# Kernel tuning notes

Hardware: AMD Instinct MI355X
Metric: run time of the kernel (lower is better)

## Reference

```python
import jax, jax.numpy as jnp
import numpy as np

C = 512
K = 3
DIL = 1
EPS = 1e-6


def weight_quant(w):
    # BitNet b1.58 ternary quantization with straight-through estimator:
    # scale = mean(|w|); w_q = clamp(round(w/scale), -1, 1) * scale
    s = jnp.maximum(jnp.mean(jnp.abs(w)), 1e-5)
    q = jnp.clip(jnp.round(w / s), -1.0, 1.0) * s
    return w + jax.lax.stop_gradient(q - w)


def conv1d(x, w, b, padding, dilation):
    # x: [B, C, L], w: [O, I, K]
    y = jax.lax.conv_general_dilated(
        x, w, window_strides=(1,), padding=[(padding, padding)],
        rhs_dilation=(dilation,), dimension_numbers=("NCH", "OIH", "NCH"))
    return y + b[None, :, None]


def setup_inputs() -> dict:
    key = jax.random.key(0)
    k0, k1, k2, k3, k4 = jax.random.split(key, 5)
    fan_in = C * K
    lim = 1.0 / np.sqrt(fan_in)
    x = jax.random.normal(k0, (16, C, 4096), dtype=jnp.float32)
    w1 = jax.random.uniform(k1, (C, C, K), jnp.float32, -lim, lim)
    b1 = jax.random.uniform(k2, (C,), jnp.float32, -lim, lim)
    w2 = jax.random.uniform(k3, (C, C, K), jnp.float32, -lim, lim)
    b2 = jax.random.uniform(k4, (C,), jnp.float32, -lim, lim)
    g = jnp.ones((C,), dtype=jnp.float32)  # RMSNorm gain
    return {"x": x, "w1": w1, "b1": b1, "w2": w2, "b2": b2, "g": g}


def reference(x, w1, b1, w2, b2, g):
    residual = x
    # RMSNorm over channel axis (original transposes to [B,L,C], norms last dim)
    ms = jnp.mean(jnp.square(x), axis=1, keepdims=True)
    h = x * jax.lax.rsqrt(ms + EPS) * g[None, :, None]
    h = jax.nn.silu(h)
    p1 = (K * DIL - DIL) // 2
    h = conv1d(h, weight_quant(w1), b1, p1, DIL)
    h = jax.nn.silu(h)
    h = conv1d(h, weight_quant(w2), b2, K // 2, 1)
    return h + residual
```

## Files before the change

kernel.cpp:

```cpp
#include <hip/hip_runtime.h>

#define BATCH 16
#define CCH 512
#define LEN 4096
#define LPAD 4098

typedef unsigned short u16;
typedef __bf16 bf16x8 __attribute__((ext_vector_type(8)));
typedef float f32x4 __attribute__((ext_vector_type(4)));
typedef u16 u16x8 __attribute__((ext_vector_type(8)));
typedef u16 u16x4 __attribute__((ext_vector_type(4)));

__device__ __forceinline__ u16 f2bf(float f) {
    unsigned u = __float_as_uint(f);
    u = (u + 0x7fffu + ((u >> 16) & 1u)) >> 16;
    return (u16)u;
}
__device__ __forceinline__ float bf2f(u16 v) {
    return __uint_as_float(((unsigned)v) << 16);
}
__device__ __forceinline__ float silu_f(float v) {
    return v / (1.f + __expf(-v));
}
__device__ __forceinline__ void async16(const u16* g, u16* l) {
    __builtin_amdgcn_global_load_lds(
        (const __attribute__((address_space(1))) unsigned int*)g,
        (__attribute__((address_space(3))) unsigned int*)l, 16, 0, 0);
}

#define SBAR() __builtin_amdgcn_sched_barrier(0)
#define HWBAR() { SBAR(); __builtin_amdgcn_s_barrier(); SBAR(); }
#define WAIT_LGKM0() { asm volatile("s_waitcnt lgkmcnt(0)" ::: "memory"); SBAR(); }
#define WAIT_VM(n) { asm volatile("s_waitcnt vmcnt(" #n ")" ::: "memory"); SBAR(); }

__global__ __launch_bounds__(256)
void absmean_partial(const float* __restrict__ w1, const float* __restrict__ w2,
                     float* __restrict__ part) {
    const int tid = threadIdx.x;
    const int base = blockIdx.x * 3072;
    float s1 = 0.f, s2 = 0.f;
    for (int i = tid; i < 3072; i += 256) {
        s1 += fabsf(w1[base + i]);
        s2 += fabsf(w2[base + i]);
    }
    __shared__ float r1[256], r2[256];
    r1[tid] = s1; r2[tid] = s2;
    __syncthreads();
    for (int off = 128; off > 0; off >>= 1) {
        if (tid < off) { r1[tid] += r1[tid + off]; r2[tid] += r2[tid + off]; }
        __syncthreads();
    }
    if (tid == 0) { part[blockIdx.x] = r1[0]; part[256 + blockIdx.x] = r2[0]; }
}

__global__ __launch_bounds__(256)
void finalize_scale(const float* __restrict__ part, float* __restrict__ sv) {
    const int tid = threadIdx.x;
    __shared__ float r1[256], r2[256];
    r1[tid] = part[tid]; r2[tid] = part[256 + tid];
    __syncthreads();
    for (int off = 128; off > 0; off >>= 1) {
        if (tid < off) { r1[tid] += r1[tid + off]; r2[tid] += r2[tid + off]; }
        __syncthreads();
    }
    if (tid == 0) {
        sv[0] = fmaxf(r1[0] * (1.f / 786432.f), 1e-5f);
        sv[1] = fmaxf(r2[0] * (1.f / 786432.f), 1e-5f);
    }
}

__global__ __launch_bounds__(256)
void quantize_w(const float* __restrict__ w, const float* __restrict__ sv,
                int sidx, u16* __restrict__ wqt) {
    const int idx = blockIdx.x * 256 + threadIdx.x;
    const float s = sv[sidx];
    float q = rintf(w[idx] / s);
    q = fmaxf(-1.f, fminf(1.f, q));
    const int o   = idx / 1536;
    const int rem = idx - o * 1536;
    const int i   = rem / 3;
    const int k   = rem - i * 3;
    wqt[k * (CCH * CCH) + o * CCH + i] = f2bf(q);
}

__global__ __launch_bounds__(256)
void zero_pads(u16* __restrict__ h, u16* __restrict__ h1) {
    const int idx = blockIdx.x * 256 + threadIdx.x;
    const int b = idx >> 10;
    const int r = (idx >> 9) & 1;
    const int i = idx & 511;
    const size_t off = ((size_t)b * LPAD + (r ? (LPAD - 1) : 0)) * CCH + i;
    h[off] = 0;
    h1[off] = 0;
}

__global__ __launch_bounds__(256)
void rms_silu_transpose(const float* __restrict__ x, const float* __restrict__ g,
                        u16* __restrict__ h_t) {
    __shared__ u16   xt[CCH][33];
    __shared__ float red[8][32];
    __shared__ float rinv[32];
    const int tid = threadIdx.x;
    const int bb  = blockIdx.x >> 7;
    const int l0  = (blockIdx.x & 127) << 5;

    const size_t xbase = (size_t)bb * CCH * LEN + l0;
    {
        const int i_hi = tid >> 3;
        const int l4   = (tid & 7) << 2;
        #pragma unroll
        for (int it = 0; it < 16; ++it) {
            const int i = it * 32 + i_hi;
            const float4 v = *(const float4*)&x[xbase + (size_t)i * LEN + l4];
            xt[i][l4 + 0] = f2bf(v.x);
            xt[i][l4 + 1] = f2bf(v.y);
            xt[i][l4 + 2] = f2bf(v.z);
            xt[i][l4 + 3] = f2bf(v.w);
        }
    }
    __syncthreads();
    {
        const int l = tid & 31, seg = tid >> 5;
        const int ibeg = seg * 64;
        float ss = 0.f;
        #pragma unroll 8
        for (int i = ibeg; i < ibeg + 64; ++i) {
            const float v = bf2f(xt[i][l]);
            ss += v * v;
        }
        red[seg][l] = ss;
    }
    __syncthreads();
    if (tid < 32) {
        float tot = 0.f;
        #pragma unroll
        for (int k2 = 0; k2 < 8; ++k2) tot += red[k2][tid];
        rinv[tid] = rsqrtf(tot * (1.f / 512.f) + 1e-6f);
    }
    __syncthreads();
    {
        const int l  = tid >> 3;
        const int i0 = (tid & 7) << 6;
        const float ri = rinv[l];
        const size_t ob = ((size_t)bb * LPAD + l0 + l + 1) * CCH + i0;
        for (int ii = 0; ii < 64; ii += 8) {
            u16x8 ov;
            #pragma unroll
            for (int jj = 0; jj < 8; ++jj) {
                const int i = i0 + ii + jj;
                float v = bf2f(xt[i][l]) * ri * g[i];
                ov[jj] = f2bf(silu_f(v));
            }
            *(u16x8*)&h_t[ob + ii] = ov;
        }
    }
}

template<int EPI>
__global__ __launch_bounds__(1024)
void conv_gemm8(const u16* __restrict__ Bsrc, const u16* __restrict__ Wq,
                const float* __restrict__ sptr, const float* __restrict__ bias,
                const float* __restrict__ resid, u16* __restrict__ outb,
                float* __restrict__ outf) {
    extern __shared__ u16 lds[];
    const int tid  = threadIdx.x;
    const int lane = tid & 63;
    const int wave = tid >> 6;
    const int wm = wave >> 2;
    const int wn = wave & 3;

    const int wgid = (blockIdx.x & 7) * 64 + (blockIdx.x >> 3);
    const int mt = wgid & 1;
    const int nt = wgid >> 1;
    const int o0 = mt << 8;
    const int bb = nt >> 4;
    const int l0 = (nt & 15) << 8;

    const int sr  = tid >> 3;
    const int scu = ((tid & 7) << 3) ^ ((sr & 7) << 3);
    const int sdst = tid << 3;

    const u16* aSrcBase = Wq + (size_t)o0 * CCH + scu;
    const u16* bSrcBase = Bsrc + ((size_t)bb * LPAD + l0) * CCH + scu;

    auto stage_full = [&](int pb, int ks2, int i02) {
        #pragma unroll
        for (int j = 0; j < 2; ++j) {
            const int r = j * 128 + sr;
            async16(aSrcBase + ks2 * (CCH * CCH) + r * CCH + i02,
                    &lds[pb * 32768 + j * 8192 + sdst]);
            async16(bSrcBase + (size_t)(r + ks2) * CCH + i02,
                    &lds[pb * 32768 + 16384 + j * 8192 + sdst]);
        }
    };

    const int swz = (lane & 7) << 3;
    const int c0 = ((lane >> 4) << 3) ^ swz;
    const int c1 = (((lane >> 4) << 3) + 32) ^ swz;
    const int aB = wm * 4096 + (lane & 15) * 64;
    const int bB = 16384 + wn * 4096 + (lane & 15) * 64;

    f32x4 acc[4][4];
    #pragma unroll
    for (int m = 0; m < 4; ++m)
        #pragma unroll
        for (int n = 0; n < 4; ++n)
            acc[m][n] = (f32x4){0.f, 0.f, 0.f, 0.f};

    stage_full(0, 0, 0);
    WAIT_VM(0);
    HWBAR();

    for (int t = 0; t < 24; ++t) {
        const int cur = t & 1;
        const int cbase = cur * 32768;
        if (t + 1 < 24) {
            const int tn = t + 1;
            stage_full(cur ^ 1, tn % 3, (tn / 3) << 6);
        }
        #pragma unroll
        for (int kk = 0; kk < 2; ++kk) {
            const int ck = kk ? c1 : c0;
            bf16x8 ar[4], br[4];
            #pragma unroll
            for (int m = 0; m < 4; ++m)
                ar[m] = *(const bf16x8*)&lds[cbase + aB + m * 1024 + ck];
            #pragma unroll
            for (int n = 0; n < 4; ++n)
                br[n] = *(const bf16x8*)&lds[cbase + bB + n * 1024 + ck];
            __builtin_amdgcn_s_setprio(1);
            #pragma unroll
            for (int m = 0; m < 4; ++m)
                #pragma unroll
                for (int n = 0; n < 4; ++n)
                    acc[m][n] = __builtin_amdgcn_mfma_f32_16x16x32_bf16(
                        ar[m], br[n], acc[m][n], 0, 0, 0);
            __builtin_amdgcn_s_setprio(0);
        }
        WAIT_LGKM0();
        WAIT_VM(0);
        HWBAR();
    }

    const float sc = sptr[0];

    if (EPI == 1) {
        #pragma unroll
        for (int m = 0; m < 4; ++m) {
            const int o_loc = wm * 64 + m * 16 + ((lane >> 4) << 2);
            const int ob = o0 + o_loc;
            const float b0 = bias[ob + 0], b1 = bias[ob + 1];
            const float b2 = bias[ob + 2], b3 = bias[ob + 3];
            #pragma unroll
            for (int n = 0; n < 4; ++n) {
                const int l_loc = wn * 64 + n * 16 + (lane & 15);
                const f32x4 a = acc[m][n];
                u16x4 ov;
                ov[0] = f2bf(silu_f(sc * a[0] + b0));
                ov[1] = f2bf(silu_f(sc * a[1] + b1));
                ov[2] = f2bf(silu_f(sc * a[2] + b2));
                ov[3] = f2bf(silu_f(sc * a[3] + b3));
                char* p = (char*)lds + l_loc * 512 +
                          (((unsigned)(o_loc << 1)) ^ ((l_loc & 7) << 4));
                *(u16x4*)p = ov;
            }
        }
        __syncthreads();
        const int l_r = tid >> 2;
        const int oq  = (tid & 3) << 3;
        u16* gdst = outb + ((size_t)bb * LPAD + l0 + l_r + 1) * CCH + o0 + oq;
        char* srp = (char*)lds + l_r * 512;
        const int swz2 = (l_r & 7) << 4;
        #pragma unroll
        for (int c = 0; c < 8; ++c) {
            const uint4 v = *(const uint4*)(srp + (((oq << 1) + c * 64) ^ swz2));
            *(uint4*)(gdst + c * 32) = v;
        }
    } else {
        const int lbase = l0 + wn * 64 + (lane & 15);
        const int obase = o0 + wm * 64 + ((lane >> 4) << 2);
        #pragma unroll
        for (int m = 0; m < 4; ++m) {
            const int ob = obase + m * 16;
            #pragma unroll
            for (int n = 0; n < 4; ++n) {
                const int l = lbase + n * 16;
                const f32x4 a = acc[m][n];
                #pragma unroll
                for (int jj = 0; jj < 4; ++jj) {
                    const size_t idx = ((size_t)bb * CCH + (ob + jj)) * LEN + l;
                    outf[idx] = sc * a[jj] + bias[ob + jj] + resid[idx];
                }
            }
        }
    }
}

extern "C" void kernel_launch(void* const* d_in, const int* in_sizes, int n_in,
                              void* d_out, int out_size, void* d_ws, size_t ws_size,
                              hipStream_t stream) {
    const float* x  = (const float*)d_in[0];
    const float* w1 = (const float*)d_in[1];
    const float* b1 = (const float*)d_in[2];
    const float* w2 = (const float*)d_in[3];
    const float* b2 = (const float*)d_in[4];
    const float* g  = (const float*)d_in[5];
    float* out = (float*)d_out;

    char* ws = (char*)d_ws;
    float* sv   = (float*)ws;
    float* part = (float*)(ws + 256);
    u16* wq1   = (u16*)(ws + 4096);
    u16* wq2   = (u16*)(ws + 4096 + 1572864);
    u16* h_t   = (u16*)(ws + 4096 + 2 * 1572864);
    u16* h1_t  = (u16*)(ws + 4096 + 2 * 1572864 + 67141632);

    hipFuncSetAttribute((const void*)conv_gemm8<1>,
                        hipFuncAttributeMaxDynamicSharedMemorySize, 131072);
    hipFuncSetAttribute((const void*)conv_gemm8<2>,
                        hipFuncAttributeMaxDynamicSharedMemorySize, 131072);

    absmean_partial<<<dim3(256), dim3(256), 0, stream>>>(w1, w2, part);
    finalize_scale<<<dim3(1), dim3(256), 0, stream>>>(part, sv);
    quantize_w<<<dim3(3072), dim3(256), 0, stream>>>(w1, sv, 0, wq1);
    quantize_w<<<dim3(3072), dim3(256), 0, stream>>>(w2, sv, 1, wq2);
    zero_pads<<<dim3(64), dim3(256), 0, stream>>>(h_t, h1_t);
    rms_silu_transpose<<<dim3(2048), dim3(256), 0, stream>>>(x, g, h_t);
    conv_gemm8<1><<<dim3(512), dim3(1024), 131072, stream>>>(h_t, wq1, sv, b1,
                                                             nullptr, h1_t, nullptr);
    conv_gemm8<2><<<dim3(512), dim3(1024), 131072, stream>>>(h1_t, wq2, sv + 1, b2,
                                                             x, nullptr, out);
}
```

Measured before the change: 306.9 us.

## Shrink conv GEMM tile to 256x128 with 3-stage async LDS pipeline

Both conv GEMM launches move from 1024-thread blocks computing 256x256 output tiles with double-buffered 64-wide K slices to 512-thread blocks computing 256x128 tiles. These now use 32-wide K slices in a triple-buffered ring, with loads issued two steps ahead. The LDS swizzle and staging pattern are rewritten to match. Dynamic LDS drops so more blocks can be resident per CU and load latency is better hidden. In exchange there are twice as many barriers per block and less operand reuse per tile.

```diff
diff --git a/kernel.cpp b/kernel.cpp
--- a/kernel.cpp
+++ b/kernel.cpp
@@ -157,7 +157,7 @@
 }
 
 template<int EPI>
-__global__ __launch_bounds__(1024)
+__global__ __launch_bounds__(512)
 void conv_gemm8(const u16* __restrict__ Bsrc, const u16* __restrict__ Wq,
                 const float* __restrict__ sptr, const float* __restrict__ bias,
                 const float* __restrict__ resid, u16* __restrict__ outb,
@@ -166,39 +166,35 @@
     const int tid  = threadIdx.x;
     const int lane = tid & 63;
     const int wave = tid >> 6;
-    const int wm = wave >> 2;
-    const int wn = wave & 3;
-
-    const int wgid = (blockIdx.x & 7) * 64 + (blockIdx.x >> 3);
+    const int wm = wave >> 1;
+    const int wn = wave & 1;
+
+    const int wgid = (blockIdx.x & 7) * 128 + (blockIdx.x >> 3);
     const int mt = wgid & 1;
     const int nt = wgid >> 1;
     const int o0 = mt << 8;
-    const int bb = nt >> 4;
-    const int l0 = (nt & 15) << 8;
-
-    const int sr  = tid >> 3;
-    const int scu = ((tid & 7) << 3) ^ ((sr & 7) << 3);
+    const int bb = nt >> 5;
+    const int l0 = (nt & 31) << 7;
+
+    const int sr   = tid >> 2;
+    const int scol = ((tid & 3) << 3) ^ ((sr & 3) << 3);
     const int sdst = tid << 3;
 
-    const u16* aSrcBase = Wq + (size_t)o0 * CCH + scu;
-    const u16* bSrcBase = Bsrc + ((size_t)bb * LPAD + l0) * CCH + scu;
-
-    auto stage_full = [&](int pb, int ks2, int i02) {
-        #pragma unroll
-        for (int j = 0; j < 2; ++j) {
-            const int r = j * 128 + sr;
-            async16(aSrcBase + ks2 * (CCH * CCH) + r * CCH + i02,
-                    &lds[pb * 32768 + j * 8192 + sdst]);
-            async16(bSrcBase + (size_t)(r + ks2) * CCH + i02,
-                    &lds[pb * 32768 + 16384 + j * 8192 + sdst]);
-        }
+    const u16* aSrcBase = Wq + (size_t)(o0 + sr) * CCH + scol;
+    const u16* bSrcBase = Bsrc + ((size_t)bb * LPAD + l0 + sr) * CCH + scol;
+
+    auto stage_full = [&](int pb, int t) {
+        const int ks = t % 3;
+        const int i0 = (t / 3) << 5;
+        const u16* wsrc = aSrcBase + ks * (CCH * CCH) + i0;
+        async16(wsrc, &lds[pb * 12288 + sdst]);
+        async16(wsrc + 128 * CCH, &lds[pb * 12288 + 4096 + sdst]);
+        async16(bSrcBase + (size_t)ks * CCH + i0, &lds[pb * 12288 + 8192 + sdst]);
     };
 
-    const int swz = (lane & 7) << 3;
-    const int c0 = ((lane >> 4) << 3) ^ swz;
-    const int c1 = (((lane >> 4) << 3) + 32) ^ swz;
-    const int aB = wm * 4096 + (lane & 15) * 64;
-    const int bB = 16384 + wn * 4096 + (lane & 15) * 64;
+    const int cc = (((lane >> 4) ^ (lane & 3)) << 3);
+    const int aOff = (wm * 64 + (lane & 15)) * 32 + cc;
+    const int bOff = 8192 + (wn * 64 + (lane & 15)) * 32 + cc;
 
     f32x4 acc[4][4];
     #pragma unroll
@@ -207,39 +203,35 @@
         for (int n = 0; n < 4; ++n)
             acc[m][n] = (f32x4){0.f, 0.f, 0.f, 0.f};
 
-    stage_full(0, 0, 0);
-    WAIT_VM(0);
+    stage_full(0, 0);
+    stage_full(1, 1);
+    WAIT_VM(3);
     HWBAR();
 
-    for (int t = 0; t < 24; ++t) {
-        const int cur = t & 1;
-        const int cbase = cur * 32768;
-        if (t + 1 < 24) {
-            const int tn = t + 1;
-            stage_full(cur ^ 1, tn % 3, (tn / 3) << 6);
-        }
-        #pragma unroll
-        for (int kk = 0; kk < 2; ++kk) {
-            const int ck = kk ? c1 : c0;
-            bf16x8 ar[4], br[4];
-            #pragma unroll
-            for (int m = 0; m < 4; ++m)
-                ar[m] = *(const bf16x8*)&lds[cbase + aB + m * 1024 + ck];
+    int pb = 0;
+    for (int t = 0; t < 48; ++t) {
+        const int cb = pb * 12288;
+        const bool full = (t < 46);
+        if (full) stage_full((pb + 2) % 3, t + 2);
+        bf16x8 ar[4], br[4];
+        #pragma unroll
+        for (int m = 0; m < 4; ++m)
+            ar[m] = *(const bf16x8*)&lds[cb + aOff + m * 512];
+        #pragma unroll
+        for (int n = 0; n < 4; ++n)
+            br[n] = *(const bf16x8*)&lds[cb + bOff + n * 512];
+        __builtin_amdgcn_s_setprio(1);
+        #pragma unroll
+        for (int m = 0; m < 4; ++m)
             #pragma unroll
             for (int n = 0; n < 4; ++n)
-                br[n] = *(const bf16x8*)&lds[cbase + bB + n * 1024 + ck];
-            __builtin_amdgcn_s_setprio(1);
-            #pragma unroll
-            for (int m = 0; m < 4; ++m)
-                #pragma unroll
-                for (int n = 0; n < 4; ++n)
-                    acc[m][n] = __builtin_amdgcn_mfma_f32_16x16x32_bf16(
-                        ar[m], br[n], acc[m][n], 0, 0, 0);
-            __builtin_amdgcn_s_setprio(0);
-        }
+                acc[m][n] = __builtin_amdgcn_mfma_f32_16x16x32_bf16(
+                    ar[m], br[n], acc[m][n], 0, 0, 0);
+        __builtin_amdgcn_s_setprio(0);
         WAIT_LGKM0();
-        WAIT_VM(0);
+        if (full) { WAIT_VM(3); } else { WAIT_VM(0); }
         HWBAR();
+        pb = (pb + 1) % 3;
     }
 
     const float sc = sptr[0];
@@ -316,9 +308,9 @@
     u16* h1_t  = (u16*)(ws + 4096 + 2 * 1572864 + 67141632);
 
     hipFuncSetAttribute((const void*)conv_gemm8<1>,
-                        hipFuncAttributeMaxDynamicSharedMemorySize, 131072);
+                        hipFuncAttributeMaxDynamicSharedMemorySize, 73728);
     hipFuncSetAttribute((const void*)conv_gemm8<2>,
-                        hipFuncAttributeMaxDynamicSharedMemorySize, 131072);
+                        hipFuncAttributeMaxDynamicSharedMemorySize, 73728);
 
     absmean_partial<<<dim3(256), dim3(256), 0, stream>>>(w1, w2, part);
     finalize_scale<<<dim3(1), dim3(256), 0, stream>>>(part, sv);
@@ -326,8 +318,8 @@
     quantize_w<<<dim3(3072), dim3(256), 0, stream>>>(w2, sv, 1, wq2);
     zero_pads<<<dim3(64), dim3(256), 0, stream>>>(h_t, h1_t);
     rms_silu_transpose<<<dim3(2048), dim3(256), 0, stream>>>(x, g, h_t);
-    conv_gemm8<1><<<dim3(512), dim3(1024), 131072, stream>>>(h_t, wq1, sv, b1,
-                                                             nullptr, h1_t, nullptr);
-    conv_gemm8<2><<<dim3(512), dim3(1024), 131072, stream>>>(h1_t, wq2, sv + 1, b2,
-                                                             x, nullptr, out);
-}
+    conv_gemm8<1><<<dim3(1024), dim3(512), 73728, stream>>>(h_t, wq1, sv, b1,
+                                                            nullptr, h1_t, nullptr);
+    conv_gemm8<2><<<dim3(1024), dim3(512), 73728, stream>>>(h1_t, wq2, sv + 1, b2,
+                                                            x, nullptr, out);
+}
```

After: 328.8 us. +7.1%, slower.

## Load weight fragments directly from global and enlarge per-wave output tile

Applied to the files above, without the earlier changes.

The conv GEMM now runs 512-thread blocks (8 waves in a 4x2 grid), and each wave computes a 64x128 tile with 32 accumulators instead of 16. The weight (A) operand is no longer staged through LDS. Each lane reads its bf16 fragments straight from global or L2 every step, and only the activation (B) tile is double-buffered in LDS. The goal is to cut LDS traffic and A-staging work and raise MFMA density per wave. The cost is higher register pressure (128 accumulator floats plus 8 B fragments) and exposed global-load latency on the A path, while the dynamic LDS request stays at 128KB.

```diff
diff --git a/kernel.cpp b/kernel.cpp
--- a/kernel.cpp
+++ b/kernel.cpp
@@ -157,8 +157,8 @@
 }
 
 template<int EPI>
-__global__ __launch_bounds__(1024)
-void conv_gemm8(const u16* __restrict__ Bsrc, const u16* __restrict__ Wq,
+__global__ __launch_bounds__(512, 2)
+void conv_gemm9(const u16* __restrict__ Bsrc, const u16* __restrict__ Wq,
                 const float* __restrict__ sptr, const float* __restrict__ bias,
                 const float* __restrict__ resid, u16* __restrict__ outb,
                 float* __restrict__ outf) {
@@ -166,8 +166,8 @@
     const int tid  = threadIdx.x;
     const int lane = tid & 63;
     const int wave = tid >> 6;
-    const int wm = wave >> 2;
-    const int wn = wave & 3;
+    const int wm = wave >> 1;
+    const int wn = wave & 1;
 
     const int wgid = (blockIdx.x & 7) * 64 + (blockIdx.x >> 3);
     const int mt = wgid & 1;
@@ -179,67 +179,68 @@
     const int sr  = tid >> 3;
     const int scu = ((tid & 7) << 3) ^ ((sr & 7) << 3);
     const int sdst = tid << 3;
-
-    const u16* aSrcBase = Wq + (size_t)o0 * CCH + scu;
-    const u16* bSrcBase = Bsrc + ((size_t)bb * LPAD + l0) * CCH + scu;
-
-    auto stage_full = [&](int pb, int ks2, int i02) {
-        #pragma unroll
-        for (int j = 0; j < 2; ++j) {
-            const int r = j * 128 + sr;
-            async16(aSrcBase + ks2 * (CCH * CCH) + r * CCH + i02,
-                    &lds[pb * 32768 + j * 8192 + sdst]);
-            async16(bSrcBase + (size_t)(r + ks2) * CCH + i02,
-                    &lds[pb * 32768 + 16384 + j * 8192 + sdst]);
-        }
+    const u16* bSrcBase = Bsrc + ((size_t)bb * LPAD + l0 + sr) * CCH + scu;
+
+    auto stageB = [&](int pb, int ks2, int i02) {
+        #pragma unroll
+        for (int j = 0; j < 4; ++j)
+            async16(bSrcBase + (size_t)(j * 64 + ks2) * CCH + i02,
+                    &lds[pb * 16384 + j * 4096 + sdst]);
     };
+
+    const u16* aLane = Wq + ((size_t)(o0 + wm * 64 + (lane & 15)) << 9) +
+                       ((lane >> 4) << 3);
 
     const int swz = (lane & 7) << 3;
     const int c0 = ((lane >> 4) << 3) ^ swz;
     const int c1 = (((lane >> 4) << 3) + 32) ^ swz;
-    const int aB = wm * 4096 + (lane & 15) * 64;
-    const int bB = 16384 + wn * 4096 + (lane & 15) * 64;
-
-    f32x4 acc[4][4];
+    const int bOffBase = (wn * 128 + (lane & 15)) * 64;
+
+    f32x4 acc[4][8];
     #pragma unroll
     for (int m = 0; m < 4; ++m)
         #pragma unroll
-        for (int n = 0; n < 4; ++n)
+        for (int n = 0; n < 8; ++n)
             acc[m][n] = (f32x4){0.f, 0.f, 0.f, 0.f};
 
-    stage_full(0, 0, 0);
+    stageB(0, 0, 0);
     WAIT_VM(0);
     HWBAR();
 
+    int ks = 0, i0 = 0;
     for (int t = 0; t < 24; ++t) {
-        const int cur = t & 1;
-        const int cbase = cur * 32768;
-        if (t + 1 < 24) {
-            const int tn = t + 1;
-            stage_full(cur ^ 1, tn % 3, (tn / 3) << 6);
-        }
+        const int pb = t & 1;
+        const u16* aT = aLane + ks * (CCH * CCH) + i0;
+        bf16x8 aA[4][2];
+        #pragma unroll
+        for (int m = 0; m < 4; ++m) {
+            aA[m][0] = *(const bf16x8*)(aT + m * 8192);
+            aA[m][1] = *(const bf16x8*)(aT + m * 8192 + 32);
+        }
+        int ksn = ks + 1, i0n = i0;
+        if (ksn == 3) { ksn = 0; i0n += 64; }
+        if (t < 23) stageB(pb ^ 1, ksn, i0n);
+        const int cb = pb * 16384;
         #pragma unroll
         for (int kk = 0; kk < 2; ++kk) {
             const int ck = kk ? c1 : c0;
-            bf16x8 ar[4], br[4];
-            #pragma unroll
-            for (int m = 0; m < 4; ++m)
-                ar[m] = *(const bf16x8*)&lds[cbase + aB + m * 1024 + ck];
-            #pragma unroll
-            for (int n = 0; n < 4; ++n)
-                br[n] = *(const bf16x8*)&lds[cbase + bB + n * 1024 + ck];
+            bf16x8 br[8];
+            #pragma unroll
+            for (int n = 0; n < 8; ++n)
+                br[n] = *(const bf16x8*)&lds[cb + bOffBase + n * 1024 + ck];
             __builtin_amdgcn_s_setprio(1);
             #pragma unroll
             for (int m = 0; m < 4; ++m)
                 #pragma unroll
-                for (int n = 0; n < 4; ++n)
+                for (int n = 0; n < 8; ++n)
                     acc[m][n] = __builtin_amdgcn_mfma_f32_16x16x32_bf16(
-                        ar[m], br[n], acc[m][n], 0, 0, 0);
+                        aA[m][kk], br[n], acc[m][n], 0, 0, 0);
             __builtin_amdgcn_s_setprio(0);
         }
         WAIT_LGKM0();
         WAIT_VM(0);
         HWBAR();
+        ks = ksn; i0 = i0n;
     }
 
     const float sc = sptr[0];
@@ -252,8 +253,8 @@
             const float b0 = bias[ob + 0], b1 = bias[ob + 1];
             const float b2 = bias[ob + 2], b3 = bias[ob + 3];
             #pragma unroll
-            for (int n = 0; n < 4; ++n) {
-                const int l_loc = wn * 64 + n * 16 + (lane & 15);
+            for (int n = 0; n < 8; ++n) {
+                const int l_loc = wn * 128 + n * 16 + (lane & 15);
                 const f32x4 a = acc[m][n];
                 u16x4 ov;
                 ov[0] = f2bf(silu_f(sc * a[0] + b0));
@@ -268,22 +269,26 @@
         __syncthreads();
         const int l_r = tid >> 2;
         const int oq  = (tid & 3) << 3;
-        u16* gdst = outb + ((size_t)bb * LPAD + l0 + l_r + 1) * CCH + o0 + oq;
-        char* srp = (char*)lds + l_r * 512;
-        const int swz2 = (l_r & 7) << 4;
-        #pragma unroll
-        for (int c = 0; c < 8; ++c) {
-            const uint4 v = *(const uint4*)(srp + (((oq << 1) + c * 64) ^ swz2));
-            *(uint4*)(gdst + c * 32) = v;
+        #pragma unroll
+        for (int pass = 0; pass < 2; ++pass) {
+            const int lr = l_r + pass * 128;
+            u16* gdst = outb + ((size_t)bb * LPAD + l0 + lr + 1) * CCH + o0 + oq;
+            char* srp = (char*)lds + lr * 512;
+            const int swz2 = (lr & 7) << 4;
+            #pragma unroll
+            for (int c = 0; c < 8; ++c) {
+                const uint4 v = *(const uint4*)(srp + (((oq << 1) + c * 64) ^ swz2));
+                *(uint4*)(gdst + c * 32) = v;
+            }
         }
     } else {
-        const int lbase = l0 + wn * 64 + (lane & 15);
+        const int lbase = l0 + wn * 128 + (lane & 15);
         const int obase = o0 + wm * 64 + ((lane >> 4) << 2);
         #pragma unroll
         for (int m = 0; m < 4; ++m) {
             const int ob = obase + m * 16;
             #pragma unroll
-            for (int n = 0; n < 4; ++n) {
+            for (int n = 0; n < 8; ++n) {
                 const int l = lbase + n * 16;
                 const f32x4 a = acc[m][n];
                 #pragma unroll
@@ -315,9 +320,9 @@
     u16* h_t   = (u16*)(ws + 4096 + 2 * 1572864);
     u16* h1_t  = (u16*)(ws + 4096 + 2 * 1572864 + 67141632);
 
-    hipFuncSetAttribute((const void*)conv_gemm8<1>,
+    hipFuncSetAttribute((const void*)conv_gemm9<1>,
                         hipFuncAttributeMaxDynamicSharedMemorySize, 131072);
-    hipFuncSetAttribute((const void*)conv_gemm8<2>,
+    hipFuncSetAttribute((const void*)conv_gemm9<2>,
                         hipFuncAttributeMaxDynamicSharedMemorySize, 131072);
 
     absmean_partial<<<dim3(256), dim3(256), 0, stream>>>(w1, w2, part);
@@ -326,8 +331,8 @@
     quantize_w<<<dim3(3072), dim3(256), 0, stream>>>(w2, sv, 1, wq2);
     zero_pads<<<dim3(64), dim3(256), 0, stream>>>(h_t, h1_t);
     rms_silu_transpose<<<dim3(2048), dim3(256), 0, stream>>>(x, g, h_t);
-    conv_gemm8<1><<<dim3(512), dim3(1024), 131072, stream>>>(h_t, wq1, sv, b1,
-                                                             nullptr, h1_t, nullptr);
-    conv_gemm8<2><<<dim3(512), dim3(1024), 131072, stream>>>(h1_t, wq2, sv + 1, b2,
-                                                             x, nullptr, out);
-}
+    conv_gemm9<1><<<dim3(512), dim3(512), 131072, stream>>>(h_t, wq1, sv, b1,
+                                                            nullptr, h1_t, nullptr);
+    conv_gemm9<2><<<dim3(512), dim3(512), 131072, stream>>>(h1_t, wq2, sv + 1, b2,
+                                                            x, nullptr, out);
+}
```

New measurement: 442.2 us. 1.44x slower.

## Switch conv GEMM to 32x32x16 MFMA tiles and fuse weight quantization launches

Applied to the files above, without the earlier changes.

The conv GEMM inner loop now uses 32x32x16 bf16 MFMA with a 2x2 f32x16 accumulator per wave instead of a 4x4 grid of 16x16x32 MFMAs. This changes the LDS fragment load pattern and both epilogue index mappings. The larger instruction is meant to cut LDS reads per FLOP and the MFMA issue count. The two weight-quantization kernels are also merged into one launch. The risks are different LDS bank-conflict behaviour under the existing swizzle and a less coalesced fp32 output store in the second epilogue.

```diff
diff --git a/kernel.cpp b/kernel.cpp
--- a/kernel.cpp
+++ b/kernel.cpp
@@ -8,6 +8,7 @@
 typedef unsigned short u16;
 typedef __bf16 bf16x8 __attribute__((ext_vector_type(8)));
 typedef float f32x4 __attribute__((ext_vector_type(4)));
+typedef float f32x16 __attribute__((ext_vector_type(16)));
 typedef u16 u16x8 __attribute__((ext_vector_type(8)));
 typedef u16 u16x4 __attribute__((ext_vector_type(4)));
 
@@ -70,17 +71,20 @@
 }
 
 __global__ __launch_bounds__(256)
-void quantize_w(const float* __restrict__ w, const float* __restrict__ sv,
-                int sidx, u16* __restrict__ wqt) {
+void quantize_both(const float* __restrict__ w1, const float* __restrict__ w2,
+                   const float* __restrict__ sv,
+                   u16* __restrict__ wq1, u16* __restrict__ wq2) {
     const int idx = blockIdx.x * 256 + threadIdx.x;
-    const float s = sv[sidx];
-    float q = rintf(w[idx] / s);
-    q = fmaxf(-1.f, fminf(1.f, q));
+    const float s1 = sv[0], s2 = sv[1];
     const int o   = idx / 1536;
     const int rem = idx - o * 1536;
     const int i   = rem / 3;
     const int k   = rem - i * 3;
-    wqt[k * (CCH * CCH) + o * CCH + i] = f2bf(q);
+    const int dst = k * (CCH * CCH) + o * CCH + i;
+    float q1 = fmaxf(-1.f, fminf(1.f, rintf(w1[idx] / s1)));
+    float q2 = fmaxf(-1.f, fminf(1.f, rintf(w2[idx] / s2)));
+    wq1[dst] = f2bf(q1);
+    wq2[dst] = f2bf(q2);
 }
 
 __global__ __launch_bounds__(256)
@@ -158,10 +162,10 @@
 
 template<int EPI>
 __global__ __launch_bounds__(1024)
-void conv_gemm8(const u16* __restrict__ Bsrc, const u16* __restrict__ Wq,
-                const float* __restrict__ sptr, const float* __restrict__ bias,
-                const float* __restrict__ resid, u16* __restrict__ outb,
-                float* __restrict__ outf) {
+void conv_gemm10(const u16* __restrict__ Bsrc, const u16* __restrict__ Wq,
+                 const float* __restrict__ sptr, const float* __restrict__ bias,
+                 const float* __restrict__ resid, u16* __restrict__ outb,
+                 float* __restrict__ outf) {
     extern __shared__ u16 lds[];
     const int tid  = threadIdx.x;
     const int lane = tid & 63;
@@ -195,74 +199,76 @@
     };
 
     const int swz = (lane & 7) << 3;
-    const int c0 = ((lane >> 4) << 3) ^ swz;
-    const int c1 = (((lane >> 4) << 3) + 32) ^ swz;
-    const int aB = wm * 4096 + (lane & 15) * 64;
-    const int bB = 16384 + wn * 4096 + (lane & 15) * 64;
-
-    f32x4 acc[4][4];
+    const int kb  = (lane >> 5) << 3;
+    const int aRowB = (wm * 64 + (lane & 31)) * 64;
+    const int bRowB = 16384 + (wn * 64 + (lane & 31)) * 64;
+
+    f32x16 acc[2][2];
     #pragma unroll
-    for (int m = 0; m < 4; ++m)
-        #pragma unroll
-        for (int n = 0; n < 4; ++n)
-            acc[m][n] = (f32x4){0.f, 0.f, 0.f, 0.f};
+    for (int m = 0; m < 2; ++m)
+        #pragma unroll
+        for (int n = 0; n < 2; ++n)
+            acc[m][n] = (f32x16){0.f,0.f,0.f,0.f,0.f,0.f,0.f,0.f,
+                                 0.f,0.f,0.f,0.f,0.f,0.f,0.f,0.f};
 
     stage_full(0, 0, 0);
     WAIT_VM(0);
     HWBAR();
 
+    int ks = 0, i0 = 0;
     for (int t = 0; t < 24; ++t) {
         const int cur = t & 1;
         const int cbase = cur * 32768;
-        if (t + 1 < 24) {
-            const int tn = t + 1;
-            stage_full(cur ^ 1, tn % 3, (tn / 3) << 6);
-        }
-        #pragma unroll
-        for (int kk = 0; kk < 2; ++kk) {
-            const int ck = kk ? c1 : c0;
-            bf16x8 ar[4], br[4];
-            #pragma unroll
-            for (int m = 0; m < 4; ++m)
-                ar[m] = *(const bf16x8*)&lds[cbase + aB + m * 1024 + ck];
-            #pragma unroll
-            for (int n = 0; n < 4; ++n)
-                br[n] = *(const bf16x8*)&lds[cbase + bB + n * 1024 + ck];
+        int ksn = ks + 1, i0n = i0;
+        if (ksn == 3) { ksn = 0; i0n += 64; }
+        if (t < 23) stage_full(cur ^ 1, ksn, i0n);
+        #pragma unroll
+        for (int s = 0; s < 4; ++s) {
+            const int ck = (s * 16 + kb) ^ swz;
+            bf16x8 av[2], bv[2];
+            #pragma unroll
+            for (int m = 0; m < 2; ++m)
+                av[m] = *(const bf16x8*)&lds[cbase + aRowB + m * 2048 + ck];
+            #pragma unroll
+            for (int n = 0; n < 2; ++n)
+                bv[n] = *(const bf16x8*)&lds[cbase + bRowB + n * 2048 + ck];
             __builtin_amdgcn_s_setprio(1);
             #pragma unroll
-            for (int m = 0; m < 4; ++m)
+            for (int m = 0; m < 2; ++m)
                 #pragma unroll
-                for (int n = 0; n < 4; ++n)
-                    acc[m][n] = __builtin_amdgcn_mfma_f32_16x16x32_bf16(
-                        ar[m], br[n], acc[m][n], 0, 0, 0);
+                for (int n = 0; n < 2; ++n)
+                    acc[m][n] = __builtin_amdgcn_mfma_f32_32x32x16_bf16(
+                        av[m], bv[n], acc[m][n], 0, 0, 0);
             __builtin_amdgcn_s_setprio(0);
         }
         WAIT_LGKM0();
         WAIT_VM(0);
         HWBAR();
+        ks = ksn; i0 = i0n;
     }
 
     const float sc = sptr[0];
+    const int hi = lane >> 5;
 
     if (EPI == 1) {
         #pragma unroll
-        for (int m = 0; m < 4; ++m) {
-            const int o_loc = wm * 64 + m * 16 + ((lane >> 4) << 2);
-            const int ob = o0 + o_loc;
-            const float b0 = bias[ob + 0], b1 = bias[ob + 1];
-            const float b2 = bias[ob + 2], b3 = bias[ob + 3];
-            #pragma unroll
-            for (int n = 0; n < 4; ++n) {
-                const int l_loc = wn * 64 + n * 16 + (lane & 15);
-                const f32x4 a = acc[m][n];
-                u16x4 ov;
-                ov[0] = f2bf(silu_f(sc * a[0] + b0));
-                ov[1] = f2bf(silu_f(sc * a[1] + b1));
-                ov[2] = f2bf(silu_f(sc * a[2] + b2));
-                ov[3] = f2bf(silu_f(sc * a[3] + b3));
-                char* p = (char*)lds + l_loc * 512 +
-                          (((unsigned)(o_loc << 1)) ^ ((l_loc & 7) << 4));
-                *(u16x4*)p = ov;
+        for (int m = 0; m < 2; ++m) {
+            #pragma unroll
+            for (int n = 0; n < 2; ++n) {
+                const int l_loc = wn * 64 + n * 32 + (lane & 31);
+                const f32x16 a = acc[m][n];
+                #pragma unroll
+                for (int q = 0; q < 4; ++q) {
+                    const int o_loc = wm * 64 + m * 32 + q * 8 + hi * 4;
+                    const int ob = o0 + o_loc;
+                    u16x4 ov;
+                    #pragma unroll
+                    for (int j = 0; j < 4; ++j)
+                        ov[j] = f2bf(silu_f(sc * a[q * 4 + j] + bias[ob + j]));
+                    char* p = (char*)lds + l_loc * 512 +
+                              (((unsigned)(o_loc << 1)) ^ ((l_loc & 7) << 4));
+                    *(u16x4*)p = ov;
+                }
             }
         }
         __syncthreads();
@@ -277,19 +283,20 @@
             *(uint4*)(gdst + c * 32) = v;
         }
     } else {
-        const int lbase = l0 + wn * 64 + (lane & 15);
-        const int obase = o0 + wm * 64 + ((lane >> 4) << 2);
-        #pragma unroll
-        for (int m = 0; m < 4; ++m) {
-            const int ob = obase + m * 16;
-            #pragma unroll
-            for (int n = 0; n < 4; ++n) {
-                const int l = lbase + n * 16;
-                const f32x4 a = acc[m][n];
+        #pragma unroll
+        for (int m = 0; m < 2; ++m) {
+            #pragma unroll
+            for (int n = 0; n < 2; ++n) {
+                const int l = l0 + wn * 64 + n * 32 + (lane & 31);
+                const f32x16 a = acc[m][n];
                 #pragma unroll
-                for (int jj = 0; jj < 4; ++jj) {
-                    const size_t idx = ((size_t)bb * CCH + (ob + jj)) * LEN + l;
-                    outf[idx] = sc * a[jj] + bias[ob + jj] + resid[idx];
+                for (int q = 0; q < 4; ++q) {
+                    const int ob = o0 + wm * 64 + m * 32 + q * 8 + hi * 4;
+                    #pragma unroll
+                    for (int j = 0; j < 4; ++j) {
+                        const size_t idx = ((size_t)bb * CCH + (ob + j)) * LEN + l;
+                        outf[idx] = sc * a[q * 4 + j] + bias[ob + j] + resid[idx];
+                    }
                 }
             }
         }
@@ -315,19 +322,18 @@
     u16* h_t   = (u16*)(ws + 4096 + 2 * 1572864);
     u16* h1_t  = (u16*)(ws + 4096 + 2 * 1572864 + 67141632);
 
-    hipFuncSetAttribute((const void*)conv_gemm8<1>,
+    hipFuncSetAttribute((const void*)conv_gemm10<1>,
                         hipFuncAttributeMaxDynamicSharedMemorySize, 131072);
-    hipFuncSetAttribute((const void*)conv_gemm8<2>,
+    hipFuncSetAttribute((const void*)conv_gemm10<2>,
                         hipFuncAttributeMaxDynamicSharedMemorySize, 131072);
 
     absmean_partial<<<dim3(256), dim3(256), 0, stream>>>(w1, w2, part);
     finalize_scale<<<dim3(1), dim3(256), 0, stream>>>(part, sv);
-    quantize_w<<<dim3(3072), dim3(256), 0, stream>>>(w1, sv, 0, wq1);
-    quantize_w<<<dim3(3072), dim3(256), 0, stream>>>(w2, sv, 1, wq2);
+    quantize_both<<<dim3(3072), dim3(256), 0, stream>>>(w1, w2, sv, wq1, wq2);
     zero_pads<<<dim3(64), dim3(256), 0, stream>>>(h_t, h1_t);
     rms_silu_transpose<<<dim3(2048), dim3(256), 0, stream>>>(x, g, h_t);
-    conv_gemm8<1><<<dim3(512), dim3(1024), 131072, stream>>>(h_t, wq1, sv, b1,
-                                                             nullptr, h1_t, nullptr);
-    conv_gemm8<2><<<dim3(512), dim3(1024), 131072, stream>>>(h1_t, wq2, sv + 1, b2,
-                                                             x, nullptr, out);
-}
+    conv_gemm10<1><<<dim3(512), dim3(1024), 131072, stream>>>(h_t, wq1, sv, b1,
+                                                              nullptr, h1_t, nullptr);
+    conv_gemm10<2><<<dim3(512), dim3(1024), 131072, stream>>>(h1_t, wq2, sv + 1, b2,
+                                                              x, nullptr, out);
+}
```

Result: slower. 332.7 us (+8.4%).
